# Performance work log

Hardware: AMD Instinct MI355X
Metric: run time of the kernel (lower is better)

Reference implementation:

```python
import jax, jax.numpy as jnp
import numpy as np

NUM_VARIABLES = 20
NUM_LAYERS = 3
NUM_CONSTRAINTS = 64
NUM_STATES = 2 ** NUM_VARIABLES
TOP_K = 10  # min(10, num_states)


def _state_bits():
    # bits[i, v] = v-th bit of i, MSB first (matches format(i, '0{n}b'))
    idx = jnp.arange(NUM_STATES, dtype=jnp.int32)
    shifts = jnp.arange(NUM_VARIABLES - 1, -1, -1, dtype=jnp.int32)
    return ((idx[:, None] >> shifts[None, :]) & 1).astype(jnp.float32)


def setup_inputs() -> dict:
    key = jax.random.key(0)
    k1, k2, k3 = jax.random.split(key, 3)
    return {
        "problem_constraints": jax.random.normal(k1, (NUM_CONSTRAINTS, NUM_VARIABLES), dtype=jnp.float32),
        "beta_params": jax.random.normal(k2, (NUM_LAYERS,), dtype=jnp.float32) * 0.1,
        "gamma_params": jax.random.normal(k3, (NUM_LAYERS,), dtype=jnp.float32) * 0.1,
    }


def reference(problem_constraints, beta_params, gamma_params):
    bits = _state_bits()  # [S, n]
    # cost_function evaluated on every basis state (vectorized over 2^n states)
    viol = bits @ problem_constraints.T  # [S, C]
    costs = jnp.sum(jnp.maximum(viol - 1.0, 0.0) ** 2, axis=1) + 0.1 * jnp.sum(bits, axis=1)
    costs = jax.lax.stop_gradient(costs)  # torch fills costs via .item(), detaching them

    amps = jnp.full((NUM_STATES,), 1.0 / np.sqrt(NUM_STATES), dtype=jnp.float32)
    for layer in range(NUM_LAYERS):
        # problem unitary: exp(-i*gamma*cost) applied to real amps, then cast back
        # to float32 (torch .to(float) keeps the real part) => multiply by cos.
        amps = amps * jnp.cos(gamma_params[layer] * costs)
        # mixer: mixed[i] = amps[i] + 0.1*sin(beta) * sum_bit amps[i ^ (1<<bit)]
        grid = amps.reshape((2,) * NUM_VARIABLES)
        nb = jnp.zeros_like(grid)
        for ax in range(NUM_VARIABLES):  # structural loop over qubit axes
            nb = nb + jnp.flip(grid, axis=ax)
        mixed = amps + 0.1 * jnp.sin(beta_params[layer]) * nb.reshape(-1)
        amps = mixed / jnp.linalg.norm(mixed)

    probs = amps ** 2  # |amplitude|^2 (amps are real after the casts)
    _, top_idx = jax.lax.top_k(probs, TOP_K)
    top_assignments = bits[top_idx]  # [K, n]
    assignment_costs = costs[top_idx]  # same formula as cost_function on each
    best = jnp.argmin(assignment_costs)
    optimal_assignment = top_assignments[best]
    optimal_cost = assignment_costs[best]
    return (optimal_assignment, optimal_cost, probs, top_assignments, assignment_costs)
```

## Files before the change

### kernel.cpp

```cpp
#include <hip/hip_runtime.h>
#include <hip/hip_fp16.h>
#include <math.h>

#define NV 20
#define NC 64
#define NSTATES (1u << 20)
#define TOPK 10
#define NB1 256
#define NCAND (NB1 * TOPK)

struct h4 { __half2 lo, hi; };

template <bool WRITEH>
__global__ __launch_bounds__(512) void k_costs(const float* __restrict__ C,
                                               float* __restrict__ costs,
                                               float* __restrict__ ph0,
                                               h4* __restrict__ ph0h,
                                               const float* __restrict__ gamma,
                                               double* __restrict__ scal,
                                               unsigned* __restrict__ ctr) {
    __shared__ float CT[17][NC];
    __shared__ float lowT[8][NC];
    const int tid = threadIdx.x;

    if (blockIdx.x == 0) {
        if (tid < 8) scal[tid] = 0.0;
        if (tid == 8) *ctr = 0u;
    }

    for (int e = tid; e < 17 * NC; e += 512) {
        int k = e / NC, c = e % NC;
        CT[k][c] = C[c * NV + (16 - k)];
    }
    for (int e = tid; e < 8 * NC; e += 512) {
        int m = e >> 6, c = e & 63;
        float v = 0.0f;
        if (m & 1) v += C[c * NV + 19];
        if (m & 2) v += C[c * NV + 18];
        if (m & 4) v += C[c * NV + 17];
        lowT[m][c] = v;
    }
    __syncthreads();

    unsigned t = blockIdx.x * 512u + (unsigned)tid;
    float g0 = gamma[0];

    float cost[8];
    #pragma unroll
    for (int s = 0; s < 8; ++s)
        cost[s] = 0.1f * (float)__popc(t * 8u + (unsigned)s);

    #pragma unroll
    for (int cc = 0; cc < 4; ++cc) {
        float4 bb[4];
        #pragma unroll
        for (int q = 0; q < 4; ++q) bb[q] = make_float4(-1.f, -1.f, -1.f, -1.f);
        #pragma unroll
        for (int k = 0; k < 17; ++k) {
            float bf = (float)((t >> k) & 1u);
            const float4* row = ((const float4*)(&CT[k][0])) + 4 * cc;
            #pragma unroll
            for (int q = 0; q < 4; ++q) {
                float4 cv = row[q];
                bb[q].x = fmaf(bf, cv.x, bb[q].x);
                bb[q].y = fmaf(bf, cv.y, bb[q].y);
                bb[q].z = fmaf(bf, cv.z, bb[q].z);
                bb[q].w = fmaf(bf, cv.w, bb[q].w);
            }
        }
        #pragma unroll
        for (int s = 0; s < 8; ++s) {
            const float4* lrow = ((const float4*)(&lowT[s][0])) + 4 * cc;
            #pragma unroll
            for (int q = 0; q < 4; ++q) {
                float4 lv = lrow[q];
                float4 v;
                v.x = bb[q].x + lv.x; v.y = bb[q].y + lv.y;
                v.z = bb[q].z + lv.z; v.w = bb[q].w + lv.w;
                float r;
                r = fmaxf(v.x, 0.f); cost[s] = fmaf(r, r, cost[s]);
                r = fmaxf(v.y, 0.f); cost[s] = fmaf(r, r, cost[s]);
                r = fmaxf(v.z, 0.f); cost[s] = fmaf(r, r, cost[s]);
                r = fmaxf(v.w, 0.f); cost[s] = fmaf(r, r, cost[s]);
            }
        }
    }

    float4* co = (float4*)(costs + (size_t)t * 8u);
    co[0] = make_float4(cost[0], cost[1], cost[2], cost[3]);
    co[1] = make_float4(cost[4], cost[5], cost[6], cost[7]);
    float ph[8];
    #pragma unroll
    for (int s = 0; s < 8; ++s) ph[s] = 0x1p-10f * cosf(g0 * cost[s]);
    float4* po = (float4*)(ph0 + (size_t)t * 8u);
    po[0] = make_float4(ph[0], ph[1], ph[2], ph[3]);
    po[1] = make_float4(ph[4], ph[5], ph[6], ph[7]);
    if (WRITEH) {
        h4 h0, h1;
        h0.lo = __floats2half2_rn(ph[0], ph[1]);
        h0.hi = __floats2half2_rn(ph[2], ph[3]);
        h1.lo = __floats2half2_rn(ph[4], ph[5]);
        h1.hi = __floats2half2_rn(ph[6], ph[7]);
        ph0h[(size_t)t * 2u + 0] = h0;
        ph0h[(size_t)t * 2u + 1] = h1;
    }
}

template <int LAYER>
__global__ __launch_bounds__(1024, 4) void k_mixh(const float* __restrict__ pin,
                                                  const h4* __restrict__ pinh,
                                                  const float* __restrict__ costs,
                                                  float* __restrict__ pout,
                                                  h4* __restrict__ pouth,
                                                  const float* __restrict__ gamma,
                                                  const float* __restrict__ beta,
                                                  double* __restrict__ scal) {
    __shared__ float4 tile[1024];
    __shared__ double dpart[16];
    const unsigned lq = threadIdx.x;
    const unsigned i4 = blockIdx.x * 1024u + lq;
    float s = 0.1f * sinf(beta[LAYER]);
    float prevscale = (LAYER == 0) ? 1.0f : (float)(1.0 / sqrt(scal[LAYER - 1]));

    float4 own = ((const float4*)pin)[i4];
    tile[lq] = own;

    h4 gv[8];
    #pragma unroll
    for (int p = 19; p >= 12; --p) gv[19 - p] = pinh[i4 ^ (1u << (p - 2))];

    __syncthreads();

    float4 nb = make_float4(0.f, 0.f, 0.f, 0.f);
    #pragma unroll
    for (int u = 0; u < 8; ++u) {
        float2 f0 = __half22float2(gv[u].lo);
        float2 f1 = __half22float2(gv[u].hi);
        nb.x += f0.x; nb.y += f0.y; nb.z += f1.x; nb.w += f1.y;
    }
    #pragma unroll
    for (int p = 11; p >= 2; --p) {
        float4 v = tile[lq ^ (1u << (p - 2))];
        nb.x += v.x; nb.y += v.y; nb.z += v.z; nb.w += v.w;
    }
    nb.x += own.z; nb.y += own.w; nb.z += own.x; nb.w += own.y;
    nb.x += own.y; nb.y += own.x; nb.z += own.w; nb.w += own.z;

    float4 m;
    m.x = prevscale * fmaf(s, nb.x, own.x);
    m.y = prevscale * fmaf(s, nb.y, own.y);
    m.z = prevscale * fmaf(s, nb.z, own.z);
    m.w = prevscale * fmaf(s, nb.w, own.w);

    float4 o;
    if (LAYER < 2) {
        float gn = gamma[LAYER + 1];
        float4 c = ((const float4*)costs)[i4];
        o.x = m.x * cosf(gn * c.x);
        o.y = m.y * cosf(gn * c.y);
        o.z = m.z * cosf(gn * c.z);
        o.w = m.w * cosf(gn * c.w);
    } else {
        o = m;
    }
    ((float4*)pout)[i4] = o;
    if (LAYER < 2) {
        h4 oh;
        oh.lo = __floats2half2_rn(o.x, o.y);
        oh.hi = __floats2half2_rn(o.z, o.w);
        pouth[i4] = oh;
    }

    double ss = (double)m.x * m.x + (double)m.y * m.y +
                (double)m.z * m.z + (double)m.w * m.w;
    #pragma unroll
    for (int off = 32; off > 0; off >>= 1) ss += __shfl_down(ss, off);
    int wid = threadIdx.x >> 6;
    if ((threadIdx.x & 63) == 0) dpart[wid] = ss;
    __syncthreads();
    if (threadIdx.x == 0) {
        double tt = 0.0;
        #pragma unroll
        for (int w = 0; w < 16; ++w) tt += dpart[w];
        atomicAdd(&scal[LAYER], tt);
    }
}

template <int LAYER, bool ALIN, bool ALOUT>
__global__ __launch_bounds__(1024, 4) void k_mix(const float* __restrict__ pin,
                                                 const float* __restrict__ costs,
                                                 float* __restrict__ pout,
                                                 const float* __restrict__ gamma,
                                                 const float* __restrict__ beta,
                                                 double* __restrict__ scal) {
    __shared__ float4 tile[1024];
    __shared__ double dpart[16];
    const unsigned lq = threadIdx.x;
    const unsigned i4 = blockIdx.x * 1024u + lq;
    float s = 0.1f * sinf(beta[LAYER]);
    float prevscale = (LAYER == 0) ? 1.0f : (float)(1.0 / sqrt(scal[LAYER - 1]));
    auto ld4 = [&](unsigned j4) -> float4 {
        if (ALIN) return ((const float4*)pin)[j4];
        float4 a;
        a.x = pin[4u * j4 + 0]; a.y = pin[4u * j4 + 1];
        a.z = pin[4u * j4 + 2]; a.w = pin[4u * j4 + 3];
        return a;
    };
    float4 own = ld4(i4);
    tile[lq] = own;
    float4 gv[8];
    #pragma unroll
    for (int p = 19; p >= 12; --p) gv[19 - p] = ld4(i4 ^ (1u << (p - 2)));
    __syncthreads();
    float4 nb = make_float4(0.f, 0.f, 0.f, 0.f);
    #pragma unroll
    for (int u = 0; u < 8; ++u) { nb.x += gv[u].x; nb.y += gv[u].y; nb.z += gv[u].z; nb.w += gv[u].w; }
    #pragma unroll
    for (int p = 11; p >= 2; --p) {
        float4 v = tile[lq ^ (1u << (p - 2))];
        nb.x += v.x; nb.y += v.y; nb.z += v.z; nb.w += v.w;
    }
    nb.x += own.z; nb.y += own.w; nb.z += own.x; nb.w += own.y;
    nb.x += own.y; nb.y += own.x; nb.z += own.w; nb.w += own.z;
    float4 m;
    m.x = prevscale * fmaf(s, nb.x, own.x);
    m.y = prevscale * fmaf(s, nb.y, own.y);
    m.z = prevscale * fmaf(s, nb.z, own.z);
    m.w = prevscale * fmaf(s, nb.w, own.w);
    float4 o;
    if (LAYER < 2) {
        float gn = gamma[LAYER + 1];
        float4 c = ((const float4*)costs)[i4];
        o.x = m.x * cosf(gn * c.x); o.y = m.y * cosf(gn * c.y);
        o.z = m.z * cosf(gn * c.z); o.w = m.w * cosf(gn * c.w);
    } else o = m;
    if (ALOUT) ((float4*)pout)[i4] = o;
    else {
        pout[4u * i4 + 0] = o.x; pout[4u * i4 + 1] = o.y;
        pout[4u * i4 + 2] = o.z; pout[4u * i4 + 3] = o.w;
    }
    double ss = (double)m.x * m.x + (double)m.y * m.y + (double)m.z * m.z + (double)m.w * m.w;
    #pragma unroll
    for (int off = 32; off > 0; off >>= 1) ss += __shfl_down(ss, off);
    int wid = threadIdx.x >> 6;
    if ((threadIdx.x & 63) == 0) dpart[wid] = ss;
    __syncthreads();
    if (threadIdx.x == 0) {
        double tt = 0.0;
        #pragma unroll
        for (int w = 0; w < 16; ++w) tt += dpart[w];
        atomicAdd(&scal[LAYER], tt);
    }
}

template <bool ALIN>
__global__ __launch_bounds__(256) void k_ptop(const float* __restrict__ A,
                                              const double* __restrict__ scal2,
                                              const float* __restrict__ costs,
                                              float* __restrict__ out,
                                              unsigned long long* __restrict__ cand,
                                              unsigned* __restrict__ ctr) {
    __shared__ unsigned long long warr[4];
    __shared__ int lastblk;
    __shared__ unsigned topi[TOPK];
    __shared__ float topc[TOPK];
    const int tid = threadIdx.x;
    float* probs_out = out + 21;
    unsigned b4 = blockIdx.x * 1024u;
    float scale = (float)(1.0 / sqrt(*scal2));

    unsigned long long k[16];
    #pragma unroll
    for (int u = 0; u < 4; ++u) {
        unsigned j4 = b4 + (unsigned)tid + 256u * u;
        float4 v;
        if (ALIN) v = ((const float4*)A)[j4];
        else {
            v.x = A[4u * j4 + 0]; v.y = A[4u * j4 + 1];
            v.z = A[4u * j4 + 2]; v.w = A[4u * j4 + 3];
        }
        float4 p;
        p.x = v.x * scale; p.x *= p.x;
        p.y = v.y * scale; p.y *= p.y;
        p.z = v.z * scale; p.z *= p.z;
        p.w = v.w * scale; p.w *= p.w;
        unsigned e0 = 4u * j4;
        probs_out[e0 + 0] = p.x; probs_out[e0 + 1] = p.y;
        probs_out[e0 + 2] = p.z; probs_out[e0 + 3] = p.w;
        k[4 * u + 0] = ((unsigned long long)__float_as_uint(p.x) << 32) | (unsigned long long)(0xFFFFFFFFu - (e0 + 0));
        k[4 * u + 1] = ((unsigned long long)__float_as_uint(p.y) << 32) | (unsigned long long)(0xFFFFFFFFu - (e0 + 1));
        k[4 * u + 2] = ((unsigned long long)__float_as_uint(p.z) << 32) | (unsigned long long)(0xFFFFFFFFu - (e0 + 2));
        k[4 * u + 3] = ((unsigned long long)__float_as_uint(p.w) << 32) | (unsigned long long)(0xFFFFFFFFu - (e0 + 3));
    }

    for (int r = 0; r < TOPK; ++r) {
        unsigned long long loc = 0ull;
        #pragma unroll
        for (int j = 0; j < 16; ++j) if (k[j] > loc) loc = k[j];
        #pragma unroll
        for (int off = 32; off > 0; off >>= 1) {
            unsigned long long o = __shfl_down(loc, off);
            if (o > loc) loc = o;
        }
        if ((tid & 63) == 0) warr[tid >> 6] = loc;
        __syncthreads();
        unsigned long long win = warr[0];
        if (warr[1] > win) win = warr[1];
        if (warr[2] > win) win = warr[2];
        if (warr[3] > win) win = warr[3];
        __syncthreads();
        #pragma unroll
        for (int j = 0; j < 16; ++j) if (k[j] == win) k[j] = 0ull;
        if (tid == 0) cand[blockIdx.x * TOPK + r] = win;
    }

    __threadfence();
    if (tid == 0) {
        unsigned old = atomicAdd(ctr, 1u);
        lastblk = (old == NB1 - 1) ? 1 : 0;
    }
    __syncthreads();
    if (!lastblk) return;
    __threadfence();

    unsigned long long c2[TOPK];
    #pragma unroll
    for (int u = 0; u < TOPK; ++u) c2[u] = cand[tid + 256 * u];

    for (int r = 0; r < TOPK; ++r) {
        unsigned long long loc = 0ull;
        #pragma unroll
        for (int u = 0; u < TOPK; ++u) if (c2[u] > loc) loc = c2[u];
        #pragma unroll
        for (int off = 32; off > 0; off >>= 1) {
            unsigned long long o = __shfl_down(loc, off);
            if (o > loc) loc = o;
        }
        if ((tid & 63) == 0) warr[tid >> 6] = loc;
        __syncthreads();
        unsigned long long win = warr[0];
        if (warr[1] > win) win = warr[1];
        if (warr[2] > win) win = warr[2];
        if (warr[3] > win) win = warr[3];
        __syncthreads();
        #pragma unroll
        for (int u = 0; u < TOPK; ++u) if (c2[u] == win) c2[u] = 0ull;
        if (tid == 0) topi[r] = 0xFFFFFFFFu - (unsigned)(win & 0xFFFFFFFFull);
        __syncthreads();
    }

    const unsigned S = NSTATES;
    if (tid < TOPK * NV) {
        int kk = tid / NV, vv = tid % NV;
        out[21 + S + (unsigned)tid] = (float)((topi[kk] >> (NV - 1 - vv)) & 1u);
    }
    if (tid < TOPK) {
        float c = costs[topi[tid]];
        topc[tid] = c;
        out[21 + S + TOPK * NV + (unsigned)tid] = c;
    }
    __syncthreads();
    if (tid == 0) {
        int best = 0;
        for (int kk = 1; kk < TOPK; ++kk)
            if (topc[kk] < topc[best]) best = kk;
        unsigned gi = topi[best];
        for (int vv = 0; vv < NV; ++vv)
            out[vv] = (float)((gi >> (NV - 1 - vv)) & 1u);
        out[NV] = topc[best];
    }
}

extern "C" void kernel_launch(void* const* d_in, const int* in_sizes, int n_in,
                              void* d_out_, int out_size, void* d_ws, size_t ws_size,
                              hipStream_t stream) {
    (void)in_sizes; (void)n_in; (void)out_size;
    const float* C     = (const float*)d_in[0];
    const float* beta  = (const float*)d_in[1];
    const float* gamma = (const float*)d_in[2];
    float* out = (float*)d_out_;
    char* ws = (char*)d_ws;
    const size_t S4 = (size_t)NSTATES * sizeof(float);
    const size_t S2 = (size_t)NSTATES * 2;

    double* scal = (double*)ws;
    unsigned* ctr = (unsigned*)(ws + 64);
    unsigned long long* cand = (unsigned long long*)(ws + 1024);
    float* costs = (float*)(ws + 32768);
    float* A     = (float*)(ws + 32768 + S4);
    float* B     = (float*)(ws + 32768 + 2 * S4);
    h4*    Ah    = (h4*)(ws + 32768 + 3 * S4);
    h4*    Bh    = (h4*)(ws + 32768 + 3 * S4 + S2);

    const size_t need_half = 32768 + 3 * S4 + 2 * S2;
    const size_t need_f32  = 32768 + 3 * S4;

    if (ws_size >= need_half) {
        k_costs<true><<<256, 512, 0, stream>>>(C, costs, A, Ah, gamma, scal, ctr);
        k_mixh<0><<<256, 1024, 0, stream>>>(A, Ah, costs, B, Bh, gamma, beta, scal);
        k_mixh<1><<<256, 1024, 0, stream>>>(B, Bh, costs, A, Ah, gamma, beta, scal);
        k_mixh<2><<<256, 1024, 0, stream>>>(A, Ah, costs, B, nullptr, gamma, beta, scal);
        k_ptop<true><<<NB1, 256, 0, stream>>>(B, scal + 2, costs, out, cand, ctr);
    } else {
        bool wsbig = (ws_size >= need_f32);
        float* Bf = wsbig ? B : (out + 21);
        k_costs<false><<<256, 512, 0, stream>>>(C, costs, A, nullptr, gamma, scal, ctr);
        if (wsbig) {
            k_mix<0, true, true ><<<256, 1024, 0, stream>>>(A, costs, Bf, gamma, beta, scal);
            k_mix<1, true, true ><<<256, 1024, 0, stream>>>(Bf, costs, A, gamma, beta, scal);
            k_mix<2, true, true ><<<256, 1024, 0, stream>>>(A, costs, Bf, gamma, beta, scal);
            k_ptop<true ><<<NB1, 256, 0, stream>>>(Bf, scal + 2, costs, out, cand, ctr);
        } else {
            k_mix<0, true, false><<<256, 1024, 0, stream>>>(A, costs, Bf, gamma, beta, scal);
            k_mix<1, false, true><<<256, 1024, 0, stream>>>(Bf, costs, A, gamma, beta, scal);
            k_mix<2, true, false><<<256, 1024, 0, stream>>>(A, costs, Bf, gamma, beta, scal);
            k_ptop<false><<<NB1, 256, 0, stream>>>(Bf, scal + 2, costs, out, cand, ctr);
        }
    }
}
```

Baseline: 84.66 us.

## Store amplitude state entirely in fp16 and double cost-kernel grid

The mixer pipeline now keeps amplitudes only in half precision. Own values, shared-memory tiles and outputs all use h4, and the fp32 copies are dropped. A new top-k kernel reads the fp16 final amplitudes. The cost kernel computes 4 states per thread over 512 blocks instead of 8 states over 256, for more parallelism. This roughly halves memory traffic per layer but adds fp16 rounding to the amplitudes, which risks probability accuracy and top-k ordering.

```diff
diff --git a/kernel.cpp b/kernel.cpp
--- a/kernel.cpp
+++ b/kernel.cpp
@@ -11,10 +11,22 @@
 
 struct h4 { __half2 lo, hi; };
 
-template <bool WRITEH>
+__device__ __forceinline__ float4 h4tof4(h4 h) {
+    float2 a = __half22float2(h.lo);
+    float2 b = __half22float2(h.hi);
+    return make_float4(a.x, a.y, b.x, b.y);
+}
+__device__ __forceinline__ h4 f4toh4(float4 v) {
+    h4 h;
+    h.lo = __floats2half2_rn(v.x, v.y);
+    h.hi = __floats2half2_rn(v.z, v.w);
+    return h;
+}
+
+template <bool WH, bool WF>
 __global__ __launch_bounds__(512) void k_costs(const float* __restrict__ C,
                                                float* __restrict__ costs,
-                                               float* __restrict__ ph0,
+                                               float* __restrict__ ph0f,
                                                h4* __restrict__ ph0h,
                                                const float* __restrict__ gamma,
                                                double* __restrict__ scal,
@@ -42,13 +54,14 @@
     }
     __syncthreads();
 
-    unsigned t = blockIdx.x * 512u + (unsigned)tid;
+    const unsigned t = blockIdx.x * 512u + (unsigned)tid;
     float g0 = gamma[0];
 
-    float cost[8];
-    #pragma unroll
-    for (int s = 0; s < 8; ++s)
-        cost[s] = 0.1f * (float)__popc(t * 8u + (unsigned)s);
+    float cost[4];
+    #pragma unroll
+    for (int s = 0; s < 4; ++s)
+        cost[s] = 0.1f * (float)__popc(4u * t + (unsigned)s);
+    const int m01 = (int)((t & 1u) << 2);
 
     #pragma unroll
     for (int cc = 0; cc < 4; ++cc) {
@@ -57,7 +70,7 @@
         for (int q = 0; q < 4; ++q) bb[q] = make_float4(-1.f, -1.f, -1.f, -1.f);
         #pragma unroll
         for (int k = 0; k < 17; ++k) {
-            float bf = (float)((t >> k) & 1u);
+            float bf = (float)((t >> (k + 1)) & 1u);
             const float4* row = ((const float4*)(&CT[k][0])) + 4 * cc;
             #pragma unroll
             for (int q = 0; q < 4; ++q) {
@@ -69,8 +82,8 @@
             }
         }
         #pragma unroll
-        for (int s = 0; s < 8; ++s) {
-            const float4* lrow = ((const float4*)(&lowT[s][0])) + 4 * cc;
+        for (int s = 0; s < 4; ++s) {
+            const float4* lrow = ((const float4*)(&lowT[m01 | s][0])) + 4 * cc;
             #pragma unroll
             for (int q = 0; q < 4; ++q) {
                 float4 lv = lrow[q];
@@ -86,44 +99,33 @@
         }
     }
 
-    float4* co = (float4*)(costs + (size_t)t * 8u);
-    co[0] = make_float4(cost[0], cost[1], cost[2], cost[3]);
-    co[1] = make_float4(cost[4], cost[5], cost[6], cost[7]);
-    float ph[8];
-    #pragma unroll
-    for (int s = 0; s < 8; ++s) ph[s] = 0x1p-10f * cosf(g0 * cost[s]);
-    float4* po = (float4*)(ph0 + (size_t)t * 8u);
-    po[0] = make_float4(ph[0], ph[1], ph[2], ph[3]);
-    po[1] = make_float4(ph[4], ph[5], ph[6], ph[7]);
-    if (WRITEH) {
-        h4 h0, h1;
-        h0.lo = __floats2half2_rn(ph[0], ph[1]);
-        h0.hi = __floats2half2_rn(ph[2], ph[3]);
-        h1.lo = __floats2half2_rn(ph[4], ph[5]);
-        h1.hi = __floats2half2_rn(ph[6], ph[7]);
-        ph0h[(size_t)t * 2u + 0] = h0;
-        ph0h[(size_t)t * 2u + 1] = h1;
-    }
+    ((float4*)costs)[t] = make_float4(cost[0], cost[1], cost[2], cost[3]);
+    float4 ph;
+    ph.x = 0x1p-10f * cosf(g0 * cost[0]);
+    ph.y = 0x1p-10f * cosf(g0 * cost[1]);
+    ph.z = 0x1p-10f * cosf(g0 * cost[2]);
+    ph.w = 0x1p-10f * cosf(g0 * cost[3]);
+    if (WH) ph0h[t] = f4toh4(ph);
+    if (WF) ((float4*)ph0f)[t] = ph;
 }
 
 template <int LAYER>
-__global__ __launch_bounds__(1024, 4) void k_mixh(const float* __restrict__ pin,
-                                                  const h4* __restrict__ pinh,
+__global__ __launch_bounds__(1024, 4) void k_mixh(const h4* __restrict__ pinh,
                                                   const float* __restrict__ costs,
-                                                  float* __restrict__ pout,
                                                   h4* __restrict__ pouth,
                                                   const float* __restrict__ gamma,
                                                   const float* __restrict__ beta,
                                                   double* __restrict__ scal) {
-    __shared__ float4 tile[1024];
+    __shared__ h4 tile[1024];
     __shared__ double dpart[16];
     const unsigned lq = threadIdx.x;
     const unsigned i4 = blockIdx.x * 1024u + lq;
     float s = 0.1f * sinf(beta[LAYER]);
     float prevscale = (LAYER == 0) ? 1.0f : (float)(1.0 / sqrt(scal[LAYER - 1]));
 
-    float4 own = ((const float4*)pin)[i4];
-    tile[lq] = own;
+    h4 ownh = pinh[i4];
+    tile[lq] = ownh;
+    float4 own = h4tof4(ownh);
 
     h4 gv[8];
     #pragma unroll
@@ -134,13 +136,12 @@
     float4 nb = make_float4(0.f, 0.f, 0.f, 0.f);
     #pragma unroll
     for (int u = 0; u < 8; ++u) {
-        float2 f0 = __half22float2(gv[u].lo);
-        float2 f1 = __half22float2(gv[u].hi);
-        nb.x += f0.x; nb.y += f0.y; nb.z += f1.x; nb.w += f1.y;
+        float4 f = h4tof4(gv[u]);
+        nb.x += f.x; nb.y += f.y; nb.z += f.z; nb.w += f.w;
     }
     #pragma unroll
     for (int p = 11; p >= 2; --p) {
-        float4 v = tile[lq ^ (1u << (p - 2))];
+        float4 v = h4tof4(tile[lq ^ (1u << (p - 2))]);
         nb.x += v.x; nb.y += v.y; nb.z += v.z; nb.w += v.w;
     }
     nb.x += own.z; nb.y += own.w; nb.z += own.x; nb.w += own.y;
@@ -163,13 +164,7 @@
     } else {
         o = m;
     }
-    ((float4*)pout)[i4] = o;
-    if (LAYER < 2) {
-        h4 oh;
-        oh.lo = __floats2half2_rn(o.x, o.y);
-        oh.hi = __floats2half2_rn(o.z, o.w);
-        pouth[i4] = oh;
-    }
+    pouth[i4] = f4toh4(o);
 
     double ss = (double)m.x * m.x + (double)m.y * m.y +
                 (double)m.z * m.z + (double)m.w * m.w;
@@ -183,6 +178,118 @@
         #pragma unroll
         for (int w = 0; w < 16; ++w) tt += dpart[w];
         atomicAdd(&scal[LAYER], tt);
+    }
+}
+
+__global__ __launch_bounds__(256) void k_ptop_h(const h4* __restrict__ Bh,
+                                                const double* __restrict__ scal2,
+                                                const float* __restrict__ costs,
+                                                float* __restrict__ out,
+                                                unsigned long long* __restrict__ cand,
+                                                unsigned* __restrict__ ctr) {
+    __shared__ unsigned long long warr[4];
+    __shared__ int lastblk;
+    __shared__ unsigned topi[TOPK];
+    __shared__ float topc[TOPK];
+    const int tid = threadIdx.x;
+    float* probs_out = out + 21;
+    unsigned b4 = blockIdx.x * 1024u;
+    float scale = (float)(1.0 / sqrt(*scal2));
+
+    unsigned long long k[16];
+    #pragma unroll
+    for (int u = 0; u < 4; ++u) {
+        unsigned j4 = b4 + (unsigned)tid + 256u * u;
+        float4 v = h4tof4(Bh[j4]);
+        float4 p;
+        p.x = v.x * scale; p.x *= p.x;
+        p.y = v.y * scale; p.y *= p.y;
+        p.z = v.z * scale; p.z *= p.z;
+        p.w = v.w * scale; p.w *= p.w;
+        unsigned e0 = 4u * j4;
+        probs_out[e0 + 0] = p.x; probs_out[e0 + 1] = p.y;
+        probs_out[e0 + 2] = p.z; probs_out[e0 + 3] = p.w;
+        k[4 * u + 0] = ((unsigned long long)__float_as_uint(p.x) << 32) | (unsigned long long)(0xFFFFFFFFu - (e0 + 0));
+        k[4 * u + 1] = ((unsigned long long)__float_as_uint(p.y) << 32) | (unsigned long long)(0xFFFFFFFFu - (e0 + 1));
+        k[4 * u + 2] = ((unsigned long long)__float_as_uint(p.z) << 32) | (unsigned long long)(0xFFFFFFFFu - (e0 + 2));
+        k[4 * u + 3] = ((unsigned long long)__float_as_uint(p.w) << 32) | (unsigned long long)(0xFFFFFFFFu - (e0 + 3));
+    }
+
+    for (int r = 0; r < TOPK; ++r) {
+        unsigned long long loc = 0ull;
+        #pragma unroll
+        for (int j = 0; j < 16; ++j) if (k[j] > loc) loc = k[j];
+        #pragma unroll
+        for (int off = 32; off > 0; off >>= 1) {
+            unsigned long long o = __shfl_down(loc, off);
+            if (o > loc) loc = o;
+        }
+        if ((tid & 63) == 0) warr[tid >> 6] = loc;
+        __syncthreads();
+        unsigned long long win = warr[0];
+        if (warr[1] > win) win = warr[1];
+        if (warr[2] > win) win = warr[2];
+        if (warr[3] > win) win = warr[3];
+        __syncthreads();
+        #pragma unroll
+        for (int j = 0; j < 16; ++j) if (k[j] == win) k[j] = 0ull;
+        if (tid == 0) cand[blockIdx.x * TOPK + r] = win;
+    }
+
+    __threadfence();
+    if (tid == 0) {
+        unsigned old = atomicAdd(ctr, 1u);
+        lastblk = (old == NB1 - 1) ? 1 : 0;
+    }
+    __syncthreads();
+    if (!lastblk) return;
+    __threadfence();
+
+    unsigned long long c2[TOPK];
+    #pragma unroll
+    for (int u = 0; u < TOPK; ++u) c2[u] = cand[tid + 256 * u];
+
+    for (int r = 0; r < TOPK; ++r) {
+        unsigned long long loc = 0ull;
+        #pragma unroll
+        for (int u = 0; u < TOPK; ++u) if (c2[u] > loc) loc = c2[u];
+        #pragma unroll
+        for (int off = 32; off > 0; off >>= 1) {
+            unsigned long long o = __shfl_down(loc, off);
+            if (o > loc) loc = o;
+        }
+        if ((tid & 63) == 0) warr[tid >> 6] = loc;
+        __syncthreads();
+        unsigned long long win = warr[0];
+        if (warr[1] > win) win = warr[1];
+        if (warr[2] > win) win = warr[2];
+        if (warr[3] > win) win = warr[3];
+        __syncthreads();
+        #pragma unroll
+        for (int u = 0; u < TOPK; ++u) if (c2[u] == win) c2[u] = 0ull;
+        if (tid == 0) topi[r] = 0xFFFFFFFFu - (unsigned)(win & 0xFFFFFFFFull);
+        __syncthreads();
+    }
+
+    const unsigned S = NSTATES;
+    if (tid < TOPK * NV) {
+        int kk = tid / NV, vv = tid % NV;
+        out[21 + S + (unsigned)tid] = (float)((topi[kk] >> (NV - 1 - vv)) & 1u);
+    }
+    if (tid < TOPK) {
+        float c = costs[topi[tid]];
+        topc[tid] = c;
+        out[21 + S + TOPK * NV + (unsigned)tid] = c;
+    }
+    __syncthreads();
+    if (tid == 0) {
+        int best = 0;
+        for (int kk = 1; kk < TOPK; ++kk)
+            if (topc[kk] < topc[best]) best = kk;
+        unsigned gi = topi[best];
+        for (int vv = 0; vv < NV; ++vv)
+            out[vv] = (float)((gi >> (NV - 1 - vv)) & 1u);
+        out[NV] = topc[best];
     }
 }
 
@@ -268,7 +375,6 @@
     float* probs_out = out + 21;
     unsigned b4 = blockIdx.x * 1024u;
     float scale = (float)(1.0 / sqrt(*scal2));
-
     unsigned long long k[16];
     #pragma unroll
     for (int u = 0; u < 4; ++u) {
@@ -292,7 +398,6 @@
         k[4 * u + 2] = ((unsigned long long)__float_as_uint(p.z) << 32) | (unsigned long long)(0xFFFFFFFFu - (e0 + 2));
         k[4 * u + 3] = ((unsigned long long)__float_as_uint(p.w) << 32) | (unsigned long long)(0xFFFFFFFFu - (e0 + 3));
     }
-
     for (int r = 0; r < TOPK; ++r) {
         unsigned long long loc = 0ull;
         #pragma unroll
@@ -313,7 +418,6 @@
         for (int j = 0; j < 16; ++j) if (k[j] == win) k[j] = 0ull;
         if (tid == 0) cand[blockIdx.x * TOPK + r] = win;
     }
-
     __threadfence();
     if (tid == 0) {
         unsigned old = atomicAdd(ctr, 1u);
@@ -322,11 +426,9 @@
     __syncthreads();
     if (!lastblk) return;
     __threadfence();
-
     unsigned long long c2[TOPK];
     #pragma unroll
     for (int u = 0; u < TOPK; ++u) c2[u] = cand[tid + 256 * u];
-
     for (int r = 0; r < TOPK; ++r) {
         unsigned long long loc = 0ull;
         #pragma unroll
@@ -348,7 +450,6 @@
         if (tid == 0) topi[r] = 0xFFFFFFFFu - (unsigned)(win & 0xFFFFFFFFull);
         __syncthreads();
     }
-
     const unsigned S = NSTATES;
     if (tid < TOPK * NV) {
         int kk = tid / NV, vv = tid % NV;
@@ -387,24 +488,25 @@
     unsigned* ctr = (unsigned*)(ws + 64);
     unsigned long long* cand = (unsigned long long*)(ws + 1024);
     float* costs = (float*)(ws + 32768);
-    float* A     = (float*)(ws + 32768 + S4);
-    float* B     = (float*)(ws + 32768 + 2 * S4);
-    h4*    Ah    = (h4*)(ws + 32768 + 3 * S4);
-    h4*    Bh    = (h4*)(ws + 32768 + 3 * S4 + S2);
-
-    const size_t need_half = 32768 + 3 * S4 + 2 * S2;
-    const size_t need_f32  = 32768 + 3 * S4;
-
-    if (ws_size >= need_half) {
-        k_costs<true><<<256, 512, 0, stream>>>(C, costs, A, Ah, gamma, scal, ctr);
-        k_mixh<0><<<256, 1024, 0, stream>>>(A, Ah, costs, B, Bh, gamma, beta, scal);
-        k_mixh<1><<<256, 1024, 0, stream>>>(B, Bh, costs, A, Ah, gamma, beta, scal);
-        k_mixh<2><<<256, 1024, 0, stream>>>(A, Ah, costs, B, nullptr, gamma, beta, scal);
-        k_ptop<true><<<NB1, 256, 0, stream>>>(B, scal + 2, costs, out, cand, ctr);
+
+    const size_t need_h = 32768 + S4 + 2 * S2;
+    const size_t need_f = 32768 + 3 * S4;
+
+    if (ws_size >= need_h) {
+        h4* Ah = (h4*)(ws + 32768 + S4);
+        h4* Bh = (h4*)(ws + 32768 + S4 + S2);
+        k_costs<true, false><<<512, 512, 0, stream>>>(C, costs, nullptr, Ah,
+                                                      gamma, scal, ctr);
+        k_mixh<0><<<256, 1024, 0, stream>>>(Ah, costs, Bh, gamma, beta, scal);
+        k_mixh<1><<<256, 1024, 0, stream>>>(Bh, costs, Ah, gamma, beta, scal);
+        k_mixh<2><<<256, 1024, 0, stream>>>(Ah, costs, Bh, gamma, beta, scal);
+        k_ptop_h<<<NB1, 256, 0, stream>>>(Bh, scal + 2, costs, out, cand, ctr);
     } else {
-        bool wsbig = (ws_size >= need_f32);
-        float* Bf = wsbig ? B : (out + 21);
-        k_costs<false><<<256, 512, 0, stream>>>(C, costs, A, nullptr, gamma, scal, ctr);
+        float* A = (float*)(ws + 32768 + S4);
+        bool wsbig = (ws_size >= need_f);
+        float* Bf = wsbig ? (float*)(ws + 32768 + 2 * S4) : (out + 21);
+        k_costs<false, true><<<512, 512, 0, stream>>>(C, costs, A, nullptr,
+                                                      gamma, scal, ctr);
         if (wsbig) {
             k_mix<0, true, true ><<<256, 1024, 0, stream>>>(A, costs, Bf, gamma, beta, scal);
             k_mix<1, true, true ><<<256, 1024, 0, stream>>>(Bf, costs, A, gamma, beta, scal);
```

Result: no change. 85.08 us (+0.5%).
